# Optimization experiments

Measured on AMD Instinct MI355X. Metric: run time of the kernel, lower is better.

## Reference

```python
import jax, jax.numpy as jnp
import numpy as np

QW_MAX = 127  # 2**(8-1) - 1


def setup_inputs() -> dict:
    key = jax.random.key(0)
    k1, k2, k3, k4, k5 = jax.random.split(key, 5)
    B, Din, H, Dout = 4096, 1024, 4096, 1024
    x = jax.random.normal(k1, (B, Din), dtype=jnp.float32)
    # float master weights (already transposed, as in quantify_weights: weight.T)
    w1f = jax.random.normal(k2, (Din, H), dtype=jnp.float32) * 0.02
    b1f = jax.random.normal(k3, (H,), dtype=jnp.float32) * 0.02
    w2f = jax.random.normal(k4, (H, Dout), dtype=jnp.float32) * 0.02
    b2f = jax.random.normal(k5, (Dout,), dtype=jnp.float32) * 0.02
    return {"x": x, "w1f": w1f, "b1f": b1f, "w2f": w2f, "b2f": b2f}


def _quantify_pair(w, b):
    # joint max-abs scale over weight and bias (matches quantify(x, x2))
    max_v = jnp.maximum(jnp.max(jnp.abs(w)), jnp.max(jnp.abs(b)))
    scale = max_v / QW_MAX
    wq = jnp.round(w / scale).astype(jnp.int8)
    bq = jnp.round(b / scale).astype(jnp.int8)
    return wq, bq, scale


def _dot_product(q_a, q_b, scale_a, scale_b, target_scale):
    # int8 GEMM with int32 accumulation, then requantize to int16
    y0 = q_a.astype(jnp.int32) @ q_b.astype(jnp.int32)  # [M, N] int32
    scale = scale_a * scale_b / target_scale
    return jnp.round(y0 * scale).astype(jnp.int16)


def reference(x, w1f, b1f, w2f, b2f):
    # weight quantization (done once at init in torch, inlined here)
    w1, b1, s1 = _quantify_pair(w1f, b1f)
    w2, b2, s2 = _quantify_pair(w2f, b2f)
    # dynamic activation quantization
    x_scale = jnp.max(jnp.abs(x)) / QW_MAX
    x_q = jnp.round(x / x_scale).astype(jnp.int8)
    # layer 1: target_scale = s1, so effective multiplier is x_scale
    o1 = _dot_product(x_q, w1, x_scale, s1, s1) + b1.astype(jnp.int16)
    # layer 2: note torch passes scale_1 (not x_scale) here — faithful to source
    o2 = _dot_product(jnp.maximum(o1, 0), w2, s1, s2, s2) + b2.astype(jnp.int16)
    # dequantize
    return o2.astype(jnp.float32) * s2
```

## Files before the change

kernel.cpp:

```cpp
#include <hip/hip_runtime.h>
#include <stdint.h>

typedef int   i32x4 __attribute__((ext_vector_type(4)));
typedef float f32x4 __attribute__((ext_vector_type(4)));

#define WS_PART    0
#define WS_XQ      32768
#define WS_W1QT    (WS_XQ   + 4096*1024)
#define WS_W2QT    (WS_W1QT + 4096*1024)
#define WS_PS      (WS_W2QT + 4096*1024)
#define WS_PH      (WS_PS   + 4096*4096)

__device__ __forceinline__ void async16(const void* g, void* l) {
  __builtin_amdgcn_global_load_lds(
      (const __attribute__((address_space(1))) unsigned*)g,
      (__attribute__((address_space(3))) unsigned*)l, 16, 0, 0);
}

__device__ __forceinline__ float block_absmax(const float* __restrict__ p0, int n0,
                                              const float* __restrict__ p1, int n1,
                                              float* red, float* slot) {
  int tid = threadIdx.x, nt = blockDim.x;
  float m = 0.f;
  for (int i = tid; i < n0; i += nt) m = fmaxf(m, fabsf(p0[i]));
  if (p1) for (int i = tid; i < n1; i += nt) m = fmaxf(m, fabsf(p1[i]));
  for (int off = 32; off; off >>= 1) m = fmaxf(m, __shfl_down(m, off));
  if ((tid & 63) == 0) red[tid >> 6] = m;
  __syncthreads();
  if (tid == 0) {
    int nw = nt >> 6;
    float M = red[0];
    for (int w = 1; w < nw; w++) M = fmaxf(M, red[w]);
    *slot = M;
  }
  __syncthreads();
  return *slot;
}

__global__ void k_absmax3(const float* __restrict__ x, const float* __restrict__ w1,
                          const float* __restrict__ w2, float* __restrict__ part) {
  int seg = blockIdx.x >> 9;
  int b = blockIdx.x & 511;
  const float* p = (seg == 0) ? x : (seg == 1) ? w1 : w2;
  int i = b * 256 + threadIdx.x;
  float m = 0.f;
  #pragma unroll
  for (int it = 0; it < 8; it++) {
    f32x4 v = ((const f32x4*)p)[i + it * 131072];
    m = fmaxf(m, fmaxf(fmaxf(fabsf(v.x), fabsf(v.y)), fmaxf(fabsf(v.z), fabsf(v.w))));
  }
  for (int off = 32; off; off >>= 1) m = fmaxf(m, __shfl_down(m, off));
  __shared__ float red[4];
  if ((threadIdx.x & 63) == 0) red[threadIdx.x >> 6] = m;
  __syncthreads();
  if (threadIdx.x == 0)
    part[blockIdx.x] = fmaxf(fmaxf(red[0], red[1]), fmaxf(red[2], red[3]));
}

__device__ __forceinline__ void quantT_body(const float* __restrict__ w, float s,
                                            i32x4* __restrict__ out, int C, int tkbits,
                                            int b) {
  int L = b * 256 + threadIdx.x;
  int h_in = L & 127;
  int kb = (L >> 7) & 3;
  int tk = (L >> 9) & ((1 << tkbits) - 1);
  int hblk = L >> (9 + tkbits);
  int h = hblk * 128 + h_in;
  int k0 = (tk * 4 + kb) * 16;
  int wd[4];
  #pragma unroll
  for (int d = 0; d < 4; d++) {
    unsigned acc = 0;
    #pragma unroll
    for (int j = 0; j < 4; j++) {
      float v = w[(size_t)(k0 + d * 4 + j) * C + h];
      int q = (int)rintf(v / s) & 255;
      acc |= (unsigned)q << (8 * j);
    }
    wd[d] = (int)acc;
  }
  i32x4 o; o.x = wd[0]; o.y = wd[1]; o.z = wd[2]; o.w = wd[3];
  out[L] = o;
}

__global__ void k_prep(const float* __restrict__ x, const float* __restrict__ w1f,
                       const float* __restrict__ w2f, const float* __restrict__ b1f,
                       const float* __restrict__ b2f, const float* __restrict__ part,
                       i32x4* __restrict__ xq, i32x4* __restrict__ w1qt,
                       i32x4* __restrict__ w2qt) {
  __shared__ float red[4];
  __shared__ float slot;
  int seg = blockIdx.x >> 10;
  int b = blockIdx.x & 1023;
  if (seg == 0) {
    float s = block_absmax(part, 512, nullptr, 0, red, &slot) / 127.0f;
    int L = b * 256 + threadIdx.x;
    int m_in = L & 127, kb = (L >> 7) & 3, tk = (L >> 9) & 15, mblk = L >> 13;
    int m = mblk * 128 + m_in;
    int k0 = (tk * 4 + kb) * 16;
    const f32x4* px = (const f32x4*)(x + m * 1024 + k0);
    int wd[4];
    #pragma unroll
    for (int d = 0; d < 4; d++) {
      f32x4 v = px[d];
      int b0 = (int)rintf(v.x / s) & 255;
      int b1 = (int)rintf(v.y / s) & 255;
      int b2 = (int)rintf(v.z / s) & 255;
      int b3 = (int)rintf(v.w / s) & 255;
      wd[d] = b0 | (b1 << 8) | (b2 << 16) | (b3 << 24);
    }
    i32x4 o; o.x = wd[0]; o.y = wd[1]; o.z = wd[2]; o.w = wd[3];
    xq[L] = o;
  } else if (seg == 1) {
    float s = block_absmax(part + 512, 512, b1f, 4096, red, &slot) / 127.0f;
    quantT_body(w1f, s, w1qt, 4096, 4, b);
  } else {
    float s = block_absmax(part + 1024, 512, b2f, 1024, red, &slot) / 127.0f;
    quantT_body(w2f, s, w2qt, 1024, 6, b);
  }
}

__launch_bounds__(256)
__global__ void k_gemm1(const i32x4* __restrict__ Aq, const i32x4* __restrict__ Bq,
                        const float* __restrict__ part, const float* __restrict__ b1f,
                        unsigned* __restrict__ plane_s, unsigned* __restrict__ plane_h) {
  __shared__ i32x4 As[2][512];
  __shared__ i32x4 Bs[2][512];
  __shared__ float red[4];
  __shared__ float slot;
  __shared__ int b1s[128];
  int tid = threadIdx.x;
  int bb = blockIdx.x;
  int hb = blockIdx.y;
  int lane = tid & 63, wid = tid >> 6;
  int wm = wid & 1, wn = wid >> 1;
  int g = lane >> 4, l15 = lane & 15;

  const i32x4* gA = Aq + (size_t)hb * 16 * 512;
  const i32x4* gB = Bq + (size_t)bb * 16 * 512;

  async16(gA + tid, &As[0][tid]);
  async16(gA + tid + 256, &As[0][tid + 256]);
  async16(gB + tid, &Bs[0][tid]);
  async16(gB + tid + 256, &Bs[0][tid + 256]);

  float sx  = block_absmax(part, 512, nullptr, 0, red, &slot) / 127.0f;
  float s1v = block_absmax(part + 512, 512, b1f, 4096, red, &slot) / 127.0f;
  float mult1 = sx * s1v / s1v;
  for (int i = tid; i < 128; i += 256)
    b1s[i] = (int)rintf(b1f[hb * 128 + i] / s1v);

  i32x4 acc[4][4];
  #pragma unroll
  for (int r = 0; r < 4; r++)
    #pragma unroll
    for (int c = 0; c < 4; c++) acc[r][c] = (i32x4)(0);

  int abase = g * 128 + wm * 64 + l15;
  int bbase = g * 128 + wn * 64 + l15;

  for (int t = 0; t < 16; ++t) {
    int cur = t & 1;
    __syncthreads();
    if (t + 1 < 16) {
      const i32x4* ga = gA + (t + 1) * 512;
      const i32x4* gb = gB + (t + 1) * 512;
      async16(ga + tid, &As[cur ^ 1][tid]);
      async16(ga + tid + 256, &As[cur ^ 1][tid + 256]);
      async16(gb + tid, &Bs[cur ^ 1][tid]);
      async16(gb + tid + 256, &Bs[cur ^ 1][tid + 256]);
    }
    i32x4 af[4], bf[4];
    #pragma unroll
    for (int r = 0; r < 4; r++) af[r] = As[cur][abase + r * 16];
    #pragma unroll
    for (int c = 0; c < 4; c++) bf[c] = Bs[cur][bbase + c * 16];
    #pragma unroll
    for (int r = 0; r < 4; r++)
      #pragma unroll
      for (int c = 0; c < 4; c++)
        acc[r][c] = __builtin_amdgcn_mfma_i32_16x16x64_i8(af[r], bf[c], acc[r][c], 0, 0, 0);
  }

  int t2base = hb * 2 + wm;
  #pragma unroll
  for (int r = 0; r < 4; r++) {
    int hloc = wm * 64 + r * 16 + 4 * g;
    int bq0 = b1s[hloc], bq1 = b1s[hloc + 1], bq2 = b1s[hloc + 2], bq3 = b1s[hloc + 3];
    #pragma unroll
    for (int c = 0; c < 4; c++) {
      unsigned lo = 0, hi = 0;
      #pragma unroll
      for (int q = 0; q < 4; q++) {
        int y0 = acc[r][c][q];
        int bqv = (q == 0) ? bq0 : (q == 1) ? bq1 : (q == 2) ? bq2 : bq3;
        int o = (short)((int)rintf((float)y0 * mult1) + bqv);
        int a = o > 0 ? o : 0;
        int s8 = (int)(signed char)(a & 0xFF);
        int h8 = (a >> 8) + (s8 < 0 ? 1 : 0);
        lo |= (unsigned)(s8 & 0xFF) << (8 * q);
        hi |= (unsigned)(h8 & 0xFF) << (8 * q);
      }
      int m_in = wn * 64 + c * 16 + l15;
      unsigned idx = (((unsigned)(bb * 64 + t2base) * 512u + (unsigned)(r * 128 + m_in)) << 2) + g;
      plane_s[idx] = lo;
      plane_h[idx] = hi;
    }
  }
}

__launch_bounds__(512)
__global__ void k_gemm2(const i32x4* __restrict__ Ps, const i32x4* __restrict__ Ph,
                        const i32x4* __restrict__ Bq, const float* __restrict__ part,
                        const float* __restrict__ b1f, const float* __restrict__ b2f,
                        float* __restrict__ out) {
  __shared__ i32x4 st[4096];
  float* red  = (float*)&st[1024];
  float* slot = red + 8;

  int tid = threadIdx.x;
  int L = blockIdx.x;
  int mb = ((L & 7) << 3) | ((L >> 3) & 7);
  int nb = L >> 6;
  int mblk = mb >> 1, half = mb & 1;
  int wid = tid >> 6, lane = tid & 63;
  int kh = wid >> 2, w2 = wid & 3;
  int wm = w2 & 1, wn = w2 >> 1;
  int g = lane >> 4, l15 = lane & 15;
  int t256 = tid & 255;
  int sbase = kh * 2048;
  int a_idx = (t256 >> 6) * 128 + half * 64 + (t256 & 63);

  {
    int t = kh * 32;
    const i32x4* pS = Ps + ((size_t)(mblk * 64 + t) << 9);
    const i32x4* pH = Ph + ((size_t)(mblk * 64 + t) << 9);
    const i32x4* pB = Bq + ((size_t)(nb * 64 + t) << 9);
    async16(pS + a_idx, &st[sbase + t256]);
    async16(pH + a_idx, &st[sbase + 256 + t256]);
    async16(pB + t256, &st[sbase + 512 + t256]);
    async16(pB + t256 + 256, &st[sbase + 768 + t256]);
  }

  float s1v = block_absmax(part + 512, 512, b1f, 4096, red, slot) / 127.0f;
  float s2v = block_absmax(part + 1024, 512, b2f, 1024, red, slot) / 127.0f;
  float mult2 = s1v * s2v / s2v;
  int bq[4];
  #pragma unroll
  for (int c = 0; c < 4; c++)
    bq[c] = (int)rintf(b2f[nb * 128 + wn * 64 + c * 16 + l15] / s2v);

  i32x4 accS[2][4], accH[2][4];
  #pragma unroll
  for (int r = 0; r < 2; r++)
    #pragma unroll
    for (int c = 0; c < 4; c++) { accS[r][c] = (i32x4)(0); accH[r][c] = (i32x4)(0); }

  for (int tt = 0; tt < 32; ++tt) {
    int cur = tt & 1;
    __syncthreads();
    if (tt + 1 < 32) {
      int t = kh * 32 + tt + 1;
      const i32x4* pS = Ps + ((size_t)(mblk * 64 + t) << 9);
      const i32x4* pH = Ph + ((size_t)(mblk * 64 + t) << 9);
      const i32x4* pB = Bq + ((size_t)(nb * 64 + t) << 9);
      int R1 = sbase + (cur ^ 1) * 1024;
      async16(pS + a_idx, &st[R1 + t256]);
      async16(pH + a_idx, &st[R1 + 256 + t256]);
      async16(pB + t256, &st[R1 + 512 + t256]);
      async16(pB + t256 + 256, &st[R1 + 768 + t256]);
    }
    int R = sbase + cur * 1024;
    i32x4 aS[2], aH[2], bf[4];
    #pragma unroll
    for (int r = 0; r < 2; r++) {
      aS[r] = st[R + g * 64 + wm * 32 + r * 16 + l15];
      aH[r] = st[R + 256 + g * 64 + wm * 32 + r * 16 + l15];
    }
    #pragma unroll
    for (int c = 0; c < 4; c++) bf[c] = st[R + 512 + g * 128 + wn * 64 + c * 16 + l15];
    #pragma unroll
    for (int r = 0; r < 2; r++)
      #pragma unroll
      for (int c = 0; c < 4; c++) {
        accS[r][c] = __builtin_amdgcn_mfma_i32_16x16x64_i8(aS[r], bf[c], accS[r][c], 0, 0, 0);
        accH[r][c] = __builtin_amdgcn_mfma_i32_16x16x64_i8(aH[r], bf[c], accH[r][c], 0, 0, 0);
      }
  }

  int y0p[2][4][4];
  #pragma unroll
  for (int r = 0; r < 2; r++)
    #pragma unroll
    for (int c = 0; c < 4; c++)
      #pragma unroll
      for (int q = 0; q < 4; q++)
        y0p[r][c][q] = accS[r][c][q] + accH[r][c][q] * 256;

  __syncthreads();
  int* mg = (int*)st;
  if (kh == 1) {
    #pragma unroll
    for (int r = 0; r < 2; r++)
      #pragma unroll
      for (int c = 0; c < 4; c++)
        #pragma unroll
        for (int q = 0; q < 4; q++)
          mg[((r * 4 + c) * 4 + q) * 256 + t256] = y0p[r][c][q];
  }
  __syncthreads();
  if (kh == 0) {
    #pragma unroll
    for (int r = 0; r < 2; r++) {
      int m0 = mb * 64 + wm * 32 + r * 16 + 4 * g;
      #pragma unroll
      for (int c = 0; c < 4; c++) {
        int n = nb * 128 + wn * 64 + c * 16 + l15;
        #pragma unroll
        for (int q = 0; q < 4; q++) {
          int y0 = y0p[r][c][q] + mg[((r * 4 + c) * 4 + q) * 256 + t256];
          int o = (short)((int)rintf((float)y0 * mult2) + bq[c]);
          out[(size_t)(m0 + q) * 1024 + n] = (float)o * s2v;
        }
      }
    }
  }
}

extern "C" void kernel_launch(void* const* d_in, const int* in_sizes, int n_in,
                              void* d_out, int out_size, void* d_ws, size_t ws_size,
                              hipStream_t stream) {
  const float* x   = (const float*)d_in[0];
  const float* w1f = (const float*)d_in[1];
  const float* b1f = (const float*)d_in[2];
  const float* w2f = (const float*)d_in[3];
  const float* b2f = (const float*)d_in[4];
  float* out = (float*)d_out;

  char* ws = (char*)d_ws;
  float*  part    = (float*)(ws + WS_PART);
  i32x4*  xq      = (i32x4*)(ws + WS_XQ);
  i32x4*  w1qt    = (i32x4*)(ws + WS_W1QT);
  i32x4*  w2qt    = (i32x4*)(ws + WS_W2QT);
  unsigned* ps    = (unsigned*)(ws + WS_PS);
  unsigned* ph    = (unsigned*)(ws + WS_PH);

  k_absmax3<<<1536, 256, 0, stream>>>(x, w1f, w2f, part);
  k_prep<<<3072, 256, 0, stream>>>(x, w1f, w2f, b1f, b2f, part, xq, w1qt, w2qt);
  k_gemm1<<<dim3(32, 32), 256, 0, stream>>>(w1qt, xq, part, b1f, ps, ph);
  k_gemm2<<<512, 512, 0, stream>>>((const i32x4*)ps, (const i32x4*)ph, w2qt,
                                   part, b1f, b2f, out);
}
```

Measured before the change: 178.3 us.

## Load B fragments directly to registers in both GEMMs, shrink LDS footprint

Both int8 GEMM kernels now fetch their B operand straight from global memory into registers, prefetching the next K step into bnext, instead of staging it through double-buffered LDS. This halves the shared memory each block uses and moves the barrier to the end of each iteration. Launch bounds now request four blocks per CU. The aim is higher occupancy and less LDS traffic, at the cost of more VGPRs and uncoalesced or redundant global loads of B across waves that share it.

```diff
diff --git a/kernel.cpp b/kernel.cpp
--- a/kernel.cpp
+++ b/kernel.cpp
@@ -120,12 +120,11 @@
   }
 }
 
-__launch_bounds__(256)
+__launch_bounds__(256, 4)
 __global__ void k_gemm1(const i32x4* __restrict__ Aq, const i32x4* __restrict__ Bq,
                         const float* __restrict__ part, const float* __restrict__ b1f,
                         unsigned* __restrict__ plane_s, unsigned* __restrict__ plane_h) {
   __shared__ i32x4 As[2][512];
-  __shared__ i32x4 Bs[2][512];
   __shared__ float red[4];
   __shared__ float slot;
   __shared__ int b1s[128];
@@ -139,10 +138,14 @@
   const i32x4* gA = Aq + (size_t)hb * 16 * 512;
   const i32x4* gB = Bq + (size_t)bb * 16 * 512;
 
+  int abase = g * 128 + wm * 64 + l15;
+  int bbase = g * 128 + wn * 64 + l15;
+
   async16(gA + tid, &As[0][tid]);
   async16(gA + tid + 256, &As[0][tid + 256]);
-  async16(gB + tid, &Bs[0][tid]);
-  async16(gB + tid + 256, &Bs[0][tid + 256]);
+  i32x4 bnow[4], bnext[4];
+  #pragma unroll
+  for (int c = 0; c < 4; c++) bnow[c] = gB[bbase + c * 16];
 
   float sx  = block_absmax(part, 512, nullptr, 0, red, &slot) / 127.0f;
   float s1v = block_absmax(part + 512, 512, b1f, 4096, red, &slot) / 127.0f;
@@ -156,30 +159,27 @@
     #pragma unroll
     for (int c = 0; c < 4; c++) acc[r][c] = (i32x4)(0);
 
-  int abase = g * 128 + wm * 64 + l15;
-  int bbase = g * 128 + wn * 64 + l15;
-
   for (int t = 0; t < 16; ++t) {
     int cur = t & 1;
-    __syncthreads();
     if (t + 1 < 16) {
       const i32x4* ga = gA + (t + 1) * 512;
       const i32x4* gb = gB + (t + 1) * 512;
       async16(ga + tid, &As[cur ^ 1][tid]);
       async16(ga + tid + 256, &As[cur ^ 1][tid + 256]);
-      async16(gb + tid, &Bs[cur ^ 1][tid]);
-      async16(gb + tid + 256, &Bs[cur ^ 1][tid + 256]);
-    }
-    i32x4 af[4], bf[4];
+      #pragma unroll
+      for (int c = 0; c < 4; c++) bnext[c] = gb[bbase + c * 16];
+    }
+    i32x4 af[4];
     #pragma unroll
     for (int r = 0; r < 4; r++) af[r] = As[cur][abase + r * 16];
     #pragma unroll
-    for (int c = 0; c < 4; c++) bf[c] = Bs[cur][bbase + c * 16];
-    #pragma unroll
     for (int r = 0; r < 4; r++)
       #pragma unroll
       for (int c = 0; c < 4; c++)
-        acc[r][c] = __builtin_amdgcn_mfma_i32_16x16x64_i8(af[r], bf[c], acc[r][c], 0, 0, 0);
+        acc[r][c] = __builtin_amdgcn_mfma_i32_16x16x64_i8(af[r], bnow[c], acc[r][c], 0, 0, 0);
+    #pragma unroll
+    for (int c = 0; c < 4; c++) bnow[c] = bnext[c];
+    __syncthreads();
   }
 
   int t2base = hb * 2 + wm;
@@ -209,14 +209,14 @@
   }
 }
 
-__launch_bounds__(512)
+__launch_bounds__(512, 4)
 __global__ void k_gemm2(const i32x4* __restrict__ Ps, const i32x4* __restrict__ Ph,
                         const i32x4* __restrict__ Bq, const float* __restrict__ part,
                         const float* __restrict__ b1f, const float* __restrict__ b2f,
                         float* __restrict__ out) {
-  __shared__ i32x4 st[4096];
-  float* red  = (float*)&st[1024];
-  float* slot = red + 8;
+  __shared__ i32x4 st[2048];
+  __shared__ float red[8];
+  __shared__ float slot;
 
   int tid = threadIdx.x;
   int L = blockIdx.x;
@@ -228,22 +228,23 @@
   int wm = w2 & 1, wn = w2 >> 1;
   int g = lane >> 4, l15 = lane & 15;
   int t256 = tid & 255;
-  int sbase = kh * 2048;
+  int khbase = kh * 1024;
   int a_idx = (t256 >> 6) * 128 + half * 64 + (t256 & 63);
-
-  {
-    int t = kh * 32;
-    const i32x4* pS = Ps + ((size_t)(mblk * 64 + t) << 9);
-    const i32x4* pH = Ph + ((size_t)(mblk * 64 + t) << 9);
-    const i32x4* pB = Bq + ((size_t)(nb * 64 + t) << 9);
-    async16(pS + a_idx, &st[sbase + t256]);
-    async16(pH + a_idx, &st[sbase + 256 + t256]);
-    async16(pB + t256, &st[sbase + 512 + t256]);
-    async16(pB + t256 + 256, &st[sbase + 768 + t256]);
-  }
-
-  float s1v = block_absmax(part + 512, 512, b1f, 4096, red, slot) / 127.0f;
-  float s2v = block_absmax(part + 1024, 512, b2f, 1024, red, slot) / 127.0f;
+  int abase = g * 64 + wm * 32 + l15;
+  int bbase = g * 128 + wn * 64 + l15;
+
+  const i32x4* gS = Ps + (((size_t)mblk * 64 + kh * 32) << 9);
+  const i32x4* gH = Ph + (((size_t)mblk * 64 + kh * 32) << 9);
+  const i32x4* gB = Bq + (((size_t)nb * 64 + kh * 32) << 9);
+
+  async16(gS + a_idx, &st[khbase + t256]);
+  async16(gH + a_idx, &st[khbase + 256 + t256]);
+  i32x4 bnow[4], bnext[4];
+  #pragma unroll
+  for (int c = 0; c < 4; c++) bnow[c] = gB[bbase + c * 16];
+
+  float s1v = block_absmax(part + 512, 512, b1f, 4096, red, &slot) / 127.0f;
+  float s2v = block_absmax(part + 1024, 512, b2f, 1024, red, &slot) / 127.0f;
   float mult2 = s1v * s2v / s2v;
   int bq[4];
   #pragma unroll
@@ -258,46 +259,35 @@
 
   for (int tt = 0; tt < 32; ++tt) {
     int cur = tt & 1;
-    __syncthreads();
     if (tt + 1 < 32) {
-      int t = kh * 32 + tt + 1;
-      const i32x4* pS = Ps + ((size_t)(mblk * 64 + t) << 9);
-      const i32x4* pH = Ph + ((size_t)(mblk * 64 + t) << 9);
-      const i32x4* pB = Bq + ((size_t)(nb * 64 + t) << 9);
-      int R1 = sbase + (cur ^ 1) * 1024;
+      const i32x4* pS = gS + ((size_t)(tt + 1) << 9);
+      const i32x4* pH = gH + ((size_t)(tt + 1) << 9);
+      const i32x4* pB = gB + ((size_t)(tt + 1) << 9);
+      int R1 = khbase + (cur ^ 1) * 512;
       async16(pS + a_idx, &st[R1 + t256]);
       async16(pH + a_idx, &st[R1 + 256 + t256]);
-      async16(pB + t256, &st[R1 + 512 + t256]);
-      async16(pB + t256 + 256, &st[R1 + 768 + t256]);
-    }
-    int R = sbase + cur * 1024;
-    i32x4 aS[2], aH[2], bf[4];
+      #pragma unroll
+      for (int c = 0; c < 4; c++) bnext[c] = pB[bbase + c * 16];
+    }
+    int R = khbase + cur * 512;
+    i32x4 aS[2], aH[2];
     #pragma unroll
     for (int r = 0; r < 2; r++) {
-      aS[r] = st[R + g * 64 + wm * 32 + r * 16 + l15];
-      aH[r] = st[R + 256 + g * 64 + wm * 32 + r * 16 + l15];
-    }
-    #pragma unroll
-    for (int c = 0; c < 4; c++) bf[c] = st[R + 512 + g * 128 + wn * 64 + c * 16 + l15];
+      aS[r] = st[R + abase + r * 16];
+      aH[r] = st[R + 256 + abase + r * 16];
+    }
     #pragma unroll
     for (int r = 0; r < 2; r++)
       #pragma unroll
       for (int c = 0; c < 4; c++) {
-        accS[r][c] = __builtin_amdgcn_mfma_i32_16x16x64_i8(aS[r], bf[c], accS[r][c], 0, 0, 0);
-        accH[r][c] = __builtin_amdgcn_mfma_i32_16x16x64_i8(aH[r], bf[c], accH[r][c], 0, 0, 0);
+        accS[r][c] = __builtin_amdgcn_mfma_i32_16x16x64_i8(aS[r], bnow[c], accS[r][c], 0, 0, 0);
+        accH[r][c] = __builtin_amdgcn_mfma_i32_16x16x64_i8(aH[r], bnow[c], accH[r][c], 0, 0, 0);
       }
-  }
-
-  int y0p[2][4][4];
-  #pragma unroll
-  for (int r = 0; r < 2; r++)
-    #pragma unroll
-    for (int c = 0; c < 4; c++)
-      #pragma unroll
-      for (int q = 0; q < 4; q++)
-        y0p[r][c][q] = accS[r][c][q] + accH[r][c][q] * 256;
-
-  __syncthreads();
+    #pragma unroll
+    for (int c = 0; c < 4; c++) bnow[c] = bnext[c];
+    __syncthreads();
+  }
+
   int* mg = (int*)st;
   if (kh == 1) {
     #pragma unroll
@@ -306,7 +296,7 @@
       for (int c = 0; c < 4; c++)
         #pragma unroll
         for (int q = 0; q < 4; q++)
-          mg[((r * 4 + c) * 4 + q) * 256 + t256] = y0p[r][c][q];
+          mg[((r * 4 + c) * 4 + q) * 256 + t256] = accS[r][c][q] + accH[r][c][q] * 256;
   }
   __syncthreads();
   if (kh == 0) {
@@ -318,7 +308,8 @@
         int n = nb * 128 + wn * 64 + c * 16 + l15;
         #pragma unroll
         for (int q = 0; q < 4; q++) {
-          int y0 = y0p[r][c][q] + mg[((r * 4 + c) * 4 + q) * 256 + t256];
+          int y0 = accS[r][c][q] + accH[r][c][q] * 256
+                 + mg[((r * 4 + c) * 4 + q) * 256 + t256];
           int o = (short)((int)rintf((float)y0 * mult2) + bq[c]);
           out[(size_t)(m0 + q) * 1024 + n] = (float)o * s2v;
         }
```

New measurement: 179.5 us. No clear change (+0.6%).
